# Optimization experiments

Measured on AMD Instinct MI355X. Metric: run time of the kernel, lower is better.

The kernel has to match this reference:

```python
import jax, jax.numpy as jnp
import numpy as np

FACTOR = 5  # module default


def setup_inputs() -> dict:
    key = jax.random.key(0)
    k1, k2, k3, k4 = jax.random.split(key, 4)
    B, L, H, D = 4, 2048, 8, 64
    S = min(FACTOR * int(np.ceil(np.log(L))), L)  # sample_k = U_part = 40
    return {
        "queries": jax.random.normal(k1, (B, L, H, D), jnp.float32),
        "keys": jax.random.normal(k2, (B, L, H, D), jnp.float32),
        "values": jax.random.normal(k3, (B, L, H, D), jnp.float32),
        "index_sample": jax.random.randint(k4, (L, S), 0, L, jnp.int32),
    }


def reference(queries, keys, values, index_sample):
    # queries/keys/values: [B, L, H, D]; index_sample: [L_Q, sample_k]
    B, L_Q, H, D = queries.shape
    L_K = keys.shape[1]
    Q = jnp.transpose(queries, (0, 2, 1, 3))  # [B,H,L_Q,D]
    K = jnp.transpose(keys, (0, 2, 1, 3))     # [B,H,L_K,D]
    V = jnp.transpose(values, (0, 2, 1, 3))   # [B,H,L_V,D]

    u = min(FACTOR * int(np.ceil(np.log(L_Q))), L_Q)  # n_top

    # --- _prob_QK: sampled QK scores (gather instead of materializing K_expand) ---
    K_sample = K[:, :, index_sample, :]                       # [B,H,L_Q,S,D]
    QK_sample = jnp.einsum('bhld,bhlsd->bhls', Q, K_sample)   # [B,H,L_Q,S]
    M = QK_sample.max(-1) - QK_sample.sum(-1) / L_K           # sparsity measure [B,H,L_Q]
    M_top = jax.lax.top_k(M, u)[1]                            # [B,H,u] query indices

    Q_reduce = jnp.take_along_axis(Q, M_top[..., None], axis=2)  # [B,H,u,D]
    scale = 1.0 / np.sqrt(D)
    scores = jnp.einsum('bhud,bhkd->bhuk', Q_reduce, K) * scale  # [B,H,u,L_K]

    # --- initial context (mask_flag=True -> cumsum of V) ---
    context = jnp.cumsum(V, axis=2)                           # [B,H,L_Q,D]

    attn = jax.nn.softmax(scores, axis=-1)
    upd = jnp.einsum('bhuk,bhkd->bhud', attn, V)              # [B,H,u,D]

    bi = jnp.arange(B)[:, None, None]
    hi = jnp.arange(H)[None, :, None]
    context = context.at[bi, hi, M_top].set(upd)              # scatter selected rows

    return jnp.transpose(context, (0, 2, 1, 3))               # [B,L_Q,H,D]
```

## Files before the change

kernel.cpp:

```cpp
#include <hip/hip_runtime.h>
#include <hip/hip_bf16.h>

#define L_SEQ 2048
#define NH 8
#define DIM 64
#define SS 40
#define UU 40
#define NHD (NH * DIM)

__global__ __launch_bounds__(256) void m_kernel(const float* __restrict__ Qg,
                                                const float* __restrict__ Kg,
                                                const int* __restrict__ idx,
                                                float* __restrict__ M) {
    int B = blockIdx.x;
    int bh = B & 31;
    int l  = (B >> 5) * 4 + (threadIdx.x >> 6);
    int lane = threadIdx.x & 63;
    int b = bh >> 3, h = bh & 7;
    int g = lane >> 3, c = lane & 7;

    const float* Qp = Qg + ((size_t)(b * L_SEQ + l) * NH + h) * DIM;
    const int* ip = idx + l * SS + g;
    int ki0 = ip[0], ki1 = ip[8], ki2 = ip[16], ki3 = ip[24], ki4 = ip[32];

    float4 q0 = *(const float4*)(Qp + 4 * c);
    float4 q1 = *(const float4*)(Qp + 32 + 4 * c);

    const float* Kbase = Kg + (size_t)b * L_SEQ * NHD + (size_t)h * DIM;
    const float* r0 = Kbase + (size_t)ki0 * NHD;
    const float* r1 = Kbase + (size_t)ki1 * NHD;
    const float* r2 = Kbase + (size_t)ki2 * NHD;
    const float* r3 = Kbase + (size_t)ki3 * NHD;
    const float* r4 = Kbase + (size_t)ki4 * NHD;

    float4 a0 = *(const float4*)(r0 + 4 * c), b0 = *(const float4*)(r0 + 32 + 4 * c);
    float4 a1 = *(const float4*)(r1 + 4 * c), b1 = *(const float4*)(r1 + 32 + 4 * c);
    float4 a2 = *(const float4*)(r2 + 4 * c), b2 = *(const float4*)(r2 + 32 + 4 * c);
    float4 a3 = *(const float4*)(r3 + 4 * c), b3 = *(const float4*)(r3 + 32 + 4 * c);
    float4 a4 = *(const float4*)(r4 + 4 * c), b4 = *(const float4*)(r4 + 32 + 4 * c);

#define DOT8(ka, kb, out) { \
    float d_ = ka.x * q0.x; \
    d_ = fmaf(ka.y, q0.y, d_); d_ = fmaf(ka.z, q0.z, d_); d_ = fmaf(ka.w, q0.w, d_); \
    d_ = fmaf(kb.x, q1.x, d_); d_ = fmaf(kb.y, q1.y, d_); \
    d_ = fmaf(kb.z, q1.z, d_); d_ = fmaf(kb.w, q1.w, d_); \
    d_ += __shfl_xor(d_, 1); d_ += __shfl_xor(d_, 2); d_ += __shfl_xor(d_, 4); \
    out = d_; }

    float d0, d1, d2, d3, d4;
    DOT8(a0, b0, d0); DOT8(a1, b1, d1); DOT8(a2, b2, d2);
    DOT8(a3, b3, d3); DOT8(a4, b4, d4);
#undef DOT8

    float mx = fmaxf(fmaxf(fmaxf(d0, d1), fmaxf(d2, d3)), d4);
    float sm = d0 + d1 + d2 + d3 + d4;
    #pragma unroll
    for (int off = 8; off < 64; off <<= 1) {
        mx = fmaxf(mx, __shfl_xor(mx, off));
        sm += __shfl_xor(sm, off);
    }
    if (lane == 0) M[(size_t)bh * L_SEQ + l] = mx - sm * (1.0f / (float)L_SEQ);
}

__global__ __launch_bounds__(256) void topk_radix_kernel(const float* __restrict__ M,
                                                         int* __restrict__ Mtop) {
    __shared__ unsigned hist[256];
    __shared__ unsigned suf[256];
    __shared__ int eq_list[64];
    __shared__ unsigned sh_bin, sh_need, sh_cnt, sh_eqc;
    int bh = blockIdx.x, tid = threadIdx.x;
    const float* Mrow = M + (size_t)bh * L_SEQ;
    int base = tid * 8;

    float4 a0 = *(const float4*)(Mrow + base);
    float4 a1 = *(const float4*)(Mrow + base + 4);
    float fv[8] = {a0.x, a0.y, a0.z, a0.w, a1.x, a1.y, a1.z, a1.w};
    unsigned key[8];
    #pragma unroll
    for (int j = 0; j < 8; ++j) {
        unsigned u = __float_as_uint(fv[j]);
        key[j] = (u & 0x80000000u) ? ~u : (u | 0x80000000u);
    }

    unsigned actmask = 0xffu;
    unsigned thresh = 0;
    int need = UU;

    #pragma unroll
    for (int shift = 24; shift >= 0; shift -= 8) {
        hist[tid] = 0;
        __syncthreads();
        #pragma unroll
        for (int j = 0; j < 8; ++j)
            if ((actmask >> j) & 1u)
                atomicAdd(&hist[(key[j] >> shift) & 0xffu], 1u);
        __syncthreads();
        if (tid < 64) {
            int b0 = tid * 4;
            unsigned h0 = hist[b0], h1 = hist[b0 + 1], h2 = hist[b0 + 2], h3 = hist[b0 + 3];
            unsigned loc = h0 + h1 + h2 + h3;
            unsigned s = loc;
            #pragma unroll
            for (int off = 1; off < 64; off <<= 1) {
                unsigned o = __shfl_down(s, off, 64);
                if (tid + off < 64) s += o;
            }
            unsigned tail = s - loc;
            suf[b0 + 3] = tail;
            suf[b0 + 2] = tail + h3;
            suf[b0 + 1] = tail + h3 + h2;
            suf[b0 + 0] = tail + h3 + h2 + h1;
        }
        __syncthreads();
        {
            int sb = (int)suf[tid];
            if (sb < need && sb + (int)hist[tid] >= need) {
                sh_bin = (unsigned)tid;
                sh_need = (unsigned)(need - sb);
            }
        }
        __syncthreads();
        unsigned Bb = sh_bin;
        need = (int)sh_need;
        thresh = (thresh << 8) | Bb;
        #pragma unroll
        for (int j = 0; j < 8; ++j)
            if ((actmask >> j) & 1u)
                if (((key[j] >> shift) & 0xffu) != Bb) actmask &= ~(1u << j);
        __syncthreads();
    }

    if (tid == 0) { sh_cnt = 0; sh_eqc = 0; }
    __syncthreads();
    int* op = Mtop + bh * UU;
    #pragma unroll
    for (int j = 0; j < 8; ++j) {
        if (key[j] > thresh) {
            unsigned p = atomicAdd(&sh_cnt, 1u);
            op[p] = base + j;
        } else if (key[j] == thresh) {
            unsigned p = atomicAdd(&sh_eqc, 1u);
            if (p < 64) eq_list[p] = base + j;
        }
    }
    __syncthreads();
    unsigned cnt = sh_cnt, eqc = sh_eqc;
    if ((int)eqc == need) {
        if (tid < (unsigned)need) op[cnt + tid] = eq_list[tid];
    } else if (tid == 0) {
        if (eqc <= 64u) {
            for (int t = 0; t < need; ++t) {
                int mi = t;
                for (int j = t + 1; j < (int)eqc; ++j)
                    if (eq_list[j] < eq_list[mi]) mi = j;
                int tmp = eq_list[t]; eq_list[t] = eq_list[mi]; eq_list[mi] = tmp;
                op[cnt + t] = eq_list[t];
            }
        } else {
            int taken = 0;
            for (int i = 0; i < L_SEQ && taken < need; ++i) {
                unsigned u = __float_as_uint(Mrow[i]);
                unsigned k = (u & 0x80000000u) ? ~u : (u | 0x80000000u);
                if (k == thresh) op[cnt + taken++] = i;
            }
        }
    }
}

__global__ __launch_bounds__(256) void attn_general(
    const float* __restrict__ Qg, const float* __restrict__ Kg,
    const float* __restrict__ Vg, const int* __restrict__ Mtop,
    float* __restrict__ pm, float* __restrict__ pl, float* __restrict__ pO,
    float* __restrict__ out, int nsplit, int direct) {
    __shared__ float qs[UU * DIM];
    __shared__ float ks[64 * 68];
    __shared__ float ps[UU * 68];
    __shared__ float mm[UU], ll[UU], al[UU];
    int bx = blockIdx.x;
    int bh = bx / nsplit, sp = bx - bh * nsplit;
    int b = bh >> 3, h = bh & 7;
    int tid = threadIdx.x;
    int cpb = 32 / nsplit;
    const int* mt = Mtop + bh * UU;

    for (int i = tid; i < UU * DIM / 8; i += 256) {
        int u = i >> 3, dv = (i & 7) * 8;
        int row = mt[u];
        const float* qp = Qg + ((size_t)(b * L_SEQ + row) * NH + h) * DIM + dv;
        *(float4*)&qs[u * DIM + dv]     = *(const float4*)qp;
        *(float4*)&qs[u * DIM + dv + 4] = *(const float4*)(qp + 4);
    }
    if (tid < UU) { mm[tid] = -INFINITY; ll[tid] = 0.f; }

    int d0 = (tid & 31) * 2, ugp = tid >> 5;
    float o0[5], o1[5];
    #pragma unroll
    for (int j = 0; j < 5; ++j) { o0[j] = 0.f; o1[j] = 0.f; }

    for (int c = 0; c < cpb; ++c) {
        int k0 = (sp * cpb + c) * 64;
        if (c) __syncthreads();
        for (int i = tid; i < 64 * DIM / 8; i += 256) {
            int r = i >> 3, dv = (i & 7) * 8;
            const float* kp = Kg + ((size_t)(b * L_SEQ + k0 + r) * NH + h) * DIM + dv;
            *(float4*)&ks[r * 68 + dv]     = *(const float4*)kp;
            *(float4*)&ks[r * 68 + dv + 4] = *(const float4*)(kp + 4);
        }
        __syncthreads();

        {
            int k = tid & 63, ug = tid >> 6;
            float acc[10];
            #pragma unroll
            for (int j = 0; j < 10; ++j) acc[j] = 0.f;
            for (int d = 0; d < DIM; d += 4) {
                float4 kv = *(float4*)&ks[k * 68 + d];
                #pragma unroll
                for (int j = 0; j < 10; ++j) {
                    float4 qv = *(float4*)&qs[(ug * 10 + j) * DIM + d];
                    acc[j] = fmaf(qv.x, kv.x, acc[j]);
                    acc[j] = fmaf(qv.y, kv.y, acc[j]);
                    acc[j] = fmaf(qv.z, kv.z, acc[j]);
                    acc[j] = fmaf(qv.w, kv.w, acc[j]);
                }
            }
            #pragma unroll
            for (int j = 0; j < 10; ++j) ps[(ug * 10 + j) * 68 + k] = acc[j] * 0.125f;
        }
        __syncthreads();

        for (int i = tid; i < 64 * DIM / 8; i += 256) {
            int r = i >> 3, dv = (i & 7) * 8;
            const float* vp = Vg + ((size_t)(b * L_SEQ + k0 + r) * NH + h) * DIM + dv;
            *(float4*)&ks[r * 68 + dv]     = *(const float4*)vp;
            *(float4*)&ks[r * 68 + dv + 4] = *(const float4*)(vp + 4);
        }
        if (tid < UU) {
            float mc = -INFINITY;
            for (int k = 0; k < 64; ++k) mc = fmaxf(mc, ps[tid * 68 + k]);
            float mn = fmaxf(mm[tid], mc);
            float a = __expf(mm[tid] - mn);
            float s = 0.f;
            for (int k = 0; k < 64; ++k) {
                float e = __expf(ps[tid * 68 + k] - mn);
                ps[tid * 68 + k] = e;
                s += e;
            }
            ll[tid] = ll[tid] * a + s;
            mm[tid] = mn;
            al[tid] = a;
        }
        __syncthreads();

        {
            #pragma unroll
            for (int j = 0; j < 5; ++j) {
                float a = al[ugp * 5 + j];
                o0[j] *= a; o1[j] *= a;
            }
            for (int k = 0; k < 64; k += 4) {
                float vf0[4], vf1[4];
                #pragma unroll
                for (int kk = 0; kk < 4; ++kk) {
                    float2 vv = *(float2*)&ks[(k + kk) * 68 + d0];
                    vf0[kk] = vv.x;
                    vf1[kk] = vv.y;
                }
                #pragma unroll
                for (int j = 0; j < 5; ++j) {
                    float4 pv = *(float4*)&ps[(ugp * 5 + j) * 68 + k];
                    o0[j] = fmaf(pv.x, vf0[0], o0[j]); o1[j] = fmaf(pv.x, vf1[0], o1[j]);
                    o0[j] = fmaf(pv.y, vf0[1], o0[j]); o1[j] = fmaf(pv.y, vf1[1], o1[j]);
                    o0[j] = fmaf(pv.z, vf0[2], o0[j]); o1[j] = fmaf(pv.z, vf1[2], o1[j]);
                    o0[j] = fmaf(pv.w, vf0[3], o0[j]); o1[j] = fmaf(pv.w, vf1[3], o1[j]);
                }
            }
        }
    }

    if (!direct) {
        if (tid < UU) {
            pm[((size_t)bh * nsplit + sp) * UU + tid] = mm[tid];
            pl[((size_t)bh * nsplit + sp) * UU + tid] = ll[tid];
        }
        size_t basep = ((size_t)bh * nsplit + sp) * UU * DIM;
        #pragma unroll
        for (int j = 0; j < 5; ++j) {
            *(float2*)&pO[basep + (size_t)(ugp * 5 + j) * DIM + d0] = make_float2(o0[j], o1[j]);
        }
    } else {
        #pragma unroll
        for (int j = 0; j < 5; ++j) {
            int u = ugp * 5 + j;
            int row = mt[u];
            float inv = 1.0f / ll[u];
            size_t o = ((size_t)(b * L_SEQ + row) * NH + h) * DIM + d0;
            out[o]     = o0[j] * inv;
            out[o + 1] = o1[j] * inv;
        }
    }
}

__global__ __launch_bounds__(256) void csum8_kernel(const float* __restrict__ Vg,
                                                    float* __restrict__ cs8) {
    int wid = blockIdx.x * 4 + (threadIdx.x >> 6);
    int lane = threadIdx.x & 63;
    int c8 = wid & 255, bh = wid >> 8;
    int b = bh >> 3, h = bh & 7;
    const float* Vp = Vg + ((size_t)(b * L_SEQ + c8 * 8) * NH + h) * DIM + lane;
    float s = 0.f;
    #pragma unroll
    for (int j = 0; j < 8; ++j) s += Vp[(size_t)j * NHD];
    cs8[((size_t)bh * 256 + c8) * 64 + lane] = s;
}

__global__ __launch_bounds__(256) void prefix8_kernel(float* __restrict__ cs8) {
    __shared__ float buf[256 * 64];
    int bh = blockIdx.x, tid = threadIdx.x;
    float* g = cs8 + (size_t)bh * 16384;
    for (int it = 0; it < 16; ++it) {
        int i = it * 1024 + tid * 4;
        *(float4*)&buf[i] = *(const float4*)&g[i];
    }
    __syncthreads();
    if (tid < 64) {
        float run = 0.f;
        for (int c = 0; c < 256; ++c) {
            float t = buf[c * 64 + tid];
            buf[c * 64 + tid] = run;
            run += t;
        }
    }
    __syncthreads();
    for (int it = 0; it < 16; ++it) {
        int i = it * 1024 + tid * 4;
        *(float4*)&g[i] = *(const float4*)&buf[i];
    }
}

__global__ __launch_bounds__(256) void csum_write8_kernel(const float* __restrict__ Vg,
                                                          const float* __restrict__ cs8,
                                                          float* __restrict__ out) {
    int wid = blockIdx.x * 4 + (threadIdx.x >> 6);
    int lane = threadIdx.x & 63;
    int c8 = wid & 255, bh = wid >> 8;
    int b = bh >> 3, h = bh & 7;
    float run = cs8[((size_t)bh * 256 + c8) * 64 + lane];
    size_t off = ((size_t)(b * L_SEQ + c8 * 8) * NH + h) * DIM + lane;
    const float* Vp = Vg + off;
    float* Op = out + off;
    #pragma unroll
    for (int j = 0; j < 8; ++j) {
        run += Vp[(size_t)j * NHD];
        Op[(size_t)j * NHD] = run;
    }
}

__global__ __launch_bounds__(256) void csum_fused_kernel(const float* __restrict__ Vg,
                                                         float* __restrict__ out) {
    __shared__ float css[32 * 64];
    int bh = blockIdx.x, tid = threadIdx.x;
    int b = bh >> 3, h = bh & 7;
    int cc = tid >> 3, d8 = (tid & 7) * 8;
    size_t off = ((size_t)(b * L_SEQ + cc * 64) * NH + h) * DIM + d8;
    const float* Vp = Vg + off;
    float s[8];
    #pragma unroll
    for (int j = 0; j < 8; ++j) s[j] = 0.f;
    for (int l = 0; l < 64; ++l) {
        float4 r0 = *(const float4*)(Vp + (size_t)l * NHD);
        float4 r1 = *(const float4*)(Vp + (size_t)l * NHD + 4);
        s[0] += r0.x; s[1] += r0.y; s[2] += r0.z; s[3] += r0.w;
        s[4] += r1.x; s[5] += r1.y; s[6] += r1.z; s[7] += r1.w;
    }
    #pragma unroll
    for (int j = 0; j < 8; ++j) css[cc * 64 + d8 + j] = s[j];
    __syncthreads();
    if (tid < 64) {
        float run = 0.f;
        for (int c = 0; c < 32; ++c) {
            float t = css[c * 64 + tid];
            css[c * 64 + tid] = run;
            run += t;
        }
    }
    __syncthreads();
    float r8[8];
    #pragma unroll
    for (int j = 0; j < 8; ++j) r8[j] = css[cc * 64 + d8 + j];
    float* Op = out + off;
    for (int l = 0; l < 64; ++l) {
        float4 r0 = *(const float4*)(Vp + (size_t)l * NHD);
        float4 r1 = *(const float4*)(Vp + (size_t)l * NHD + 4);
        r8[0] += r0.x; r8[1] += r0.y; r8[2] += r0.z; r8[3] += r0.w;
        r8[4] += r1.x; r8[5] += r1.y; r8[6] += r1.z; r8[7] += r1.w;
        *(float4*)(Op + (size_t)l * NHD)     = make_float4(r8[0], r8[1], r8[2], r8[3]);
        *(float4*)(Op + (size_t)l * NHD + 4) = make_float4(r8[4], r8[5], r8[6], r8[7]);
    }
}

__global__ __launch_bounds__(256) void combine_kernel(
    const float* __restrict__ pm, const float* __restrict__ pl,
    const float* __restrict__ pO, const int* __restrict__ Mtop,
    float* __restrict__ out, int nsplit) {
    int wid = blockIdx.x * 4 + (threadIdx.x >> 6);
    int lane = threadIdx.x & 63;
    int u = wid % UU;
    int bh = wid / UU;
    int b = bh >> 3, h = bh & 7;
    float mg = -INFINITY;
    for (int c = 0; c < nsplit; ++c) mg = fmaxf(mg, pm[((size_t)bh * nsplit + c) * UU + u]);
    float acc = 0.f, lsum = 0.f;
    for (int c = 0; c < nsplit; ++c) {
        size_t pb = ((size_t)bh * nsplit + c) * UU + u;
        float w = __expf(pm[pb] - mg);
        lsum = fmaf(pl[pb], w, lsum);
        acc = fmaf(w, pO[pb * DIM + lane], acc);
    }
    int row = Mtop[bh * UU + u];
    out[((size_t)(b * L_SEQ + row) * NH + h) * DIM + lane] = acc / lsum;
}

extern "C" void kernel_launch(void* const* d_in, const int* in_sizes, int n_in,
                              void* d_out, int out_size, void* d_ws, size_t ws_size,
                              hipStream_t stream) {
    const float* Q = (const float*)d_in[0];
    const float* K = (const float*)d_in[1];
    const float* V = (const float*)d_in[2];
    const int* idx = (const int*)d_in[3];
    float* out = (float*)d_out;
    float* wsf = (float*)d_ws;

    int n = 0;
    const int cands[5] = {32, 16, 8, 4, 2};
    for (int i = 0; i < 5; ++i) {
        size_t need = (size_t)(591104 + 84480 * cands[i]) * 4;
        if (ws_size >= need) { n = cands[i]; break; }
    }

    if (n > 0) {
        float* M    = wsf;
        int*   Mtop = (int*)(wsf + 65536);
        float* pm   = wsf + 66816;
        float* pl   = pm + 1280 * (size_t)n;
        float* pO   = pl + 1280 * (size_t)n;
        float* cs8  = pO + 81920 * (size_t)n;
        m_kernel<<<16384, 256, 0, stream>>>(Q, K, idx, M);
        topk_radix_kernel<<<32, 256, 0, stream>>>(M, Mtop);
        attn_general<<<32 * n, 256, 0, stream>>>(Q, K, V, Mtop, pm, pl, pO, out, n, 0);
        csum8_kernel<<<2048, 256, 0, stream>>>(V, cs8);
        prefix8_kernel<<<32, 256, 0, stream>>>(cs8);
        csum_write8_kernel<<<2048, 256, 0, stream>>>(V, cs8, out);
        combine_kernel<<<320, 256, 0, stream>>>(pm, pl, pO, Mtop, out, n);
    } else if (ws_size >= (size_t)(66816 + 524288) * 4) {
        float* M    = wsf;
        int*   Mtop = (int*)(wsf + 65536);
        float* cs8  = wsf + 66816;
        m_kernel<<<16384, 256, 0, stream>>>(Q, K, idx, M);
        topk_radix_kernel<<<32, 256, 0, stream>>>(M, Mtop);
        csum8_kernel<<<2048, 256, 0, stream>>>(V, cs8);
        prefix8_kernel<<<32, 256, 0, stream>>>(cs8);
        csum_write8_kernel<<<2048, 256, 0, stream>>>(V, cs8, out);
        attn_general<<<32, 256, 0, stream>>>(Q, K, V, Mtop, nullptr, nullptr, nullptr, out, 1, 1);
    } else {
        float* M    = (float*)d_out;
        int*   Mtop = (int*)d_ws;
        m_kernel<<<16384, 256, 0, stream>>>(Q, K, idx, M);
        topk_radix_kernel<<<32, 256, 0, stream>>>(M, Mtop);
        csum_fused_kernel<<<32, 256, 0, stream>>>(V, out);
        attn_general<<<32, 256, 0, stream>>>(Q, K, V, Mtop, nullptr, nullptr, nullptr, out, 1, 1);
    }
}
```

Measured before the change: 191.4 us.

## Merge independent kernels into three heterogeneous stages and remap M computation

Independent work is grouped into shared launches by block-index range: M scoring with the V chunk sums, top-k selection with the chunk prefix scan, and sampled attention with the cumulative-sum write-out. This cuts the launch count from seven to four and lets independent work share the GPU. The M kernel is also remapped so each wavefront covers all 8 heads for one query position and loops over the 40 samples, giving contiguous K-row reads across heads. The cost is fewer blocks for the M stage, more serial work per wave, and larger shared-memory footprints in the combined kernels, which can lower occupancy.

```diff
diff --git a/kernel.cpp b/kernel.cpp
--- a/kernel.cpp
+++ b/kernel.cpp
@@ -1,44 +1,30 @@
 #include <hip/hip_runtime.h>
-#include <hip/hip_bf16.h>
 
 #define L_SEQ 2048
 #define NH 8
 #define DIM 64
 #define SS 40
 #define UU 40
-#define NHD (NH * DIM)
-
-__global__ __launch_bounds__(256) void m_kernel(const float* __restrict__ Qg,
-                                                const float* __restrict__ Kg,
-                                                const int* __restrict__ idx,
-                                                float* __restrict__ M) {
-    int B = blockIdx.x;
-    int bh = B & 31;
-    int l  = (B >> 5) * 4 + (threadIdx.x >> 6);
-    int lane = threadIdx.x & 63;
-    int b = bh >> 3, h = bh & 7;
-    int g = lane >> 3, c = lane & 7;
-
-    const float* Qp = Qg + ((size_t)(b * L_SEQ + l) * NH + h) * DIM;
-    const int* ip = idx + l * SS + g;
-    int ki0 = ip[0], ki1 = ip[8], ki2 = ip[16], ki3 = ip[24], ki4 = ip[32];
-
-    float4 q0 = *(const float4*)(Qp + 4 * c);
-    float4 q1 = *(const float4*)(Qp + 32 + 4 * c);
-
-    const float* Kbase = Kg + (size_t)b * L_SEQ * NHD + (size_t)h * DIM;
-    const float* r0 = Kbase + (size_t)ki0 * NHD;
-    const float* r1 = Kbase + (size_t)ki1 * NHD;
-    const float* r2 = Kbase + (size_t)ki2 * NHD;
-    const float* r3 = Kbase + (size_t)ki3 * NHD;
-    const float* r4 = Kbase + (size_t)ki4 * NHD;
-
-    float4 a0 = *(const float4*)(r0 + 4 * c), b0 = *(const float4*)(r0 + 32 + 4 * c);
-    float4 a1 = *(const float4*)(r1 + 4 * c), b1 = *(const float4*)(r1 + 32 + 4 * c);
-    float4 a2 = *(const float4*)(r2 + 4 * c), b2 = *(const float4*)(r2 + 32 + 4 * c);
-    float4 a3 = *(const float4*)(r3 + 4 * c), b3 = *(const float4*)(r3 + 32 + 4 * c);
-    float4 a4 = *(const float4*)(r4 + 4 * c), b4 = *(const float4*)(r4 + 32 + 4 * c);
-
+#define NHD 512
+
+
+__device__ __forceinline__ void m_body(const float* __restrict__ Qg,
+                                       const float* __restrict__ Kg,
+                                       const int* __restrict__ idx,
+                                       float* __restrict__ M,
+                                       int bx, int tid) {
+    int lane = tid & 63;
+    int b = bx & 3;
+    int l = (bx >> 2) * 4 + (tid >> 6);
+    int h = lane >> 3, c = lane & 7;
+
+    const float* Qp = Qg + ((size_t)(b * L_SEQ + l) * NH + h) * DIM + c * 8;
+    float4 q0 = *(const float4*)Qp;
+    float4 q1 = *(const float4*)(Qp + 4);
+    const float* Kbase = Kg + (size_t)b * L_SEQ * NHD + h * DIM + c * 8;
+    const int* ip = idx + l * SS;
+
+    float mx = -INFINITY, sm = 0.f;
 #define DOT8(ka, kb, out) { \
     float d_ = ka.x * q0.x; \
     d_ = fmaf(ka.y, q0.y, d_); d_ = fmaf(ka.z, q0.z, d_); d_ = fmaf(ka.w, q0.w, d_); \
@@ -46,140 +32,67 @@
     d_ = fmaf(kb.z, q1.z, d_); d_ = fmaf(kb.w, q1.w, d_); \
     d_ += __shfl_xor(d_, 1); d_ += __shfl_xor(d_, 2); d_ += __shfl_xor(d_, 4); \
     out = d_; }
-
-    float d0, d1, d2, d3, d4;
-    DOT8(a0, b0, d0); DOT8(a1, b1, d1); DOT8(a2, b2, d2);
-    DOT8(a3, b3, d3); DOT8(a4, b4, d4);
+    #pragma unroll
+    for (int s = 0; s < SS; s += 5) {
+        int k0 = ip[s], k1 = ip[s+1], k2 = ip[s+2], k3 = ip[s+3], k4 = ip[s+4];
+        const float* r0 = Kbase + (size_t)k0 * NHD;
+        const float* r1 = Kbase + (size_t)k1 * NHD;
+        const float* r2 = Kbase + (size_t)k2 * NHD;
+        const float* r3 = Kbase + (size_t)k3 * NHD;
+        const float* r4 = Kbase + (size_t)k4 * NHD;
+        float4 a0 = *(const float4*)r0, b0 = *(const float4*)(r0 + 4);
+        float4 a1 = *(const float4*)r1, b1 = *(const float4*)(r1 + 4);
+        float4 a2 = *(const float4*)r2, b2 = *(const float4*)(r2 + 4);
+        float4 a3 = *(const float4*)r3, b3 = *(const float4*)(r3 + 4);
+        float4 a4 = *(const float4*)r4, b4 = *(const float4*)(r4 + 4);
+        float d0, d1, d2, d3, d4;
+        DOT8(a0, b0, d0); DOT8(a1, b1, d1); DOT8(a2, b2, d2);
+        DOT8(a3, b3, d3); DOT8(a4, b4, d4);
+        mx = fmaxf(mx, fmaxf(fmaxf(d0, d1), fmaxf(fmaxf(d2, d3), d4)));
+        sm += d0 + d1 + d2 + d3 + d4;
+    }
 #undef DOT8
-
-    float mx = fmaxf(fmaxf(fmaxf(d0, d1), fmaxf(d2, d3)), d4);
-    float sm = d0 + d1 + d2 + d3 + d4;
-    #pragma unroll
-    for (int off = 8; off < 64; off <<= 1) {
-        mx = fmaxf(mx, __shfl_xor(mx, off));
-        sm += __shfl_xor(sm, off);
-    }
-    if (lane == 0) M[(size_t)bh * L_SEQ + l] = mx - sm * (1.0f / (float)L_SEQ);
-}
-
-__global__ __launch_bounds__(256) void topk_radix_kernel(const float* __restrict__ M,
-                                                         int* __restrict__ Mtop) {
-    __shared__ unsigned hist[256];
-    __shared__ unsigned suf[256];
-    __shared__ int eq_list[64];
-    __shared__ unsigned sh_bin, sh_need, sh_cnt, sh_eqc;
-    int bh = blockIdx.x, tid = threadIdx.x;
-    const float* Mrow = M + (size_t)bh * L_SEQ;
-    int base = tid * 8;
-
-    float4 a0 = *(const float4*)(Mrow + base);
-    float4 a1 = *(const float4*)(Mrow + base + 4);
-    float fv[8] = {a0.x, a0.y, a0.z, a0.w, a1.x, a1.y, a1.z, a1.w};
-    unsigned key[8];
+    if (c == 0) M[((size_t)(b * NH + h)) * L_SEQ + l] = mx - sm * (1.0f / (float)L_SEQ);
+}
+
+__device__ __forceinline__ void csum8_body(const float* __restrict__ Vg,
+                                           float* __restrict__ cs8,
+                                           int wid, int lane) {
+    int c8 = wid & 255, bh = wid >> 8;
+    int b = bh >> 3, h = bh & 7;
+    const float* Vp = Vg + ((size_t)(b * L_SEQ + c8 * 8) * NH + h) * DIM + lane;
+    float s = 0.f;
+    #pragma unroll
+    for (int j = 0; j < 8; ++j) s += Vp[(size_t)j * NHD];
+    cs8[((size_t)bh * 256 + c8) * 64 + lane] = s;
+}
+
+__device__ __forceinline__ void write8_body(const float* __restrict__ Vg,
+                                            const float* __restrict__ cs8,
+                                            float* __restrict__ out,
+                                            int wid, int lane) {
+    int c8 = wid & 255, bh = wid >> 8;
+    int b = bh >> 3, h = bh & 7;
+    float run = cs8[((size_t)bh * 256 + c8) * 64 + lane];
+    size_t off = ((size_t)(b * L_SEQ + c8 * 8) * NH + h) * DIM + lane;
+    const float* Vp = Vg + off;
+    float* Op = out + off;
     #pragma unroll
     for (int j = 0; j < 8; ++j) {
-        unsigned u = __float_as_uint(fv[j]);
-        key[j] = (u & 0x80000000u) ? ~u : (u | 0x80000000u);
-    }
-
-    unsigned actmask = 0xffu;
-    unsigned thresh = 0;
-    int need = UU;
-
-    #pragma unroll
-    for (int shift = 24; shift >= 0; shift -= 8) {
-        hist[tid] = 0;
-        __syncthreads();
-        #pragma unroll
-        for (int j = 0; j < 8; ++j)
-            if ((actmask >> j) & 1u)
-                atomicAdd(&hist[(key[j] >> shift) & 0xffu], 1u);
-        __syncthreads();
-        if (tid < 64) {
-            int b0 = tid * 4;
-            unsigned h0 = hist[b0], h1 = hist[b0 + 1], h2 = hist[b0 + 2], h3 = hist[b0 + 3];
-            unsigned loc = h0 + h1 + h2 + h3;
-            unsigned s = loc;
-            #pragma unroll
-            for (int off = 1; off < 64; off <<= 1) {
-                unsigned o = __shfl_down(s, off, 64);
-                if (tid + off < 64) s += o;
-            }
-            unsigned tail = s - loc;
-            suf[b0 + 3] = tail;
-            suf[b0 + 2] = tail + h3;
-            suf[b0 + 1] = tail + h3 + h2;
-            suf[b0 + 0] = tail + h3 + h2 + h1;
-        }
-        __syncthreads();
-        {
-            int sb = (int)suf[tid];
-            if (sb < need && sb + (int)hist[tid] >= need) {
-                sh_bin = (unsigned)tid;
-                sh_need = (unsigned)(need - sb);
-            }
-        }
-        __syncthreads();
-        unsigned Bb = sh_bin;
-        need = (int)sh_need;
-        thresh = (thresh << 8) | Bb;
-        #pragma unroll
-        for (int j = 0; j < 8; ++j)
-            if ((actmask >> j) & 1u)
-                if (((key[j] >> shift) & 0xffu) != Bb) actmask &= ~(1u << j);
-        __syncthreads();
-    }
-
-    if (tid == 0) { sh_cnt = 0; sh_eqc = 0; }
-    __syncthreads();
-    int* op = Mtop + bh * UU;
-    #pragma unroll
-    for (int j = 0; j < 8; ++j) {
-        if (key[j] > thresh) {
-            unsigned p = atomicAdd(&sh_cnt, 1u);
-            op[p] = base + j;
-        } else if (key[j] == thresh) {
-            unsigned p = atomicAdd(&sh_eqc, 1u);
-            if (p < 64) eq_list[p] = base + j;
-        }
-    }
-    __syncthreads();
-    unsigned cnt = sh_cnt, eqc = sh_eqc;
-    if ((int)eqc == need) {
-        if (tid < (unsigned)need) op[cnt + tid] = eq_list[tid];
-    } else if (tid == 0) {
-        if (eqc <= 64u) {
-            for (int t = 0; t < need; ++t) {
-                int mi = t;
-                for (int j = t + 1; j < (int)eqc; ++j)
-                    if (eq_list[j] < eq_list[mi]) mi = j;
-                int tmp = eq_list[t]; eq_list[t] = eq_list[mi]; eq_list[mi] = tmp;
-                op[cnt + t] = eq_list[t];
-            }
-        } else {
-            int taken = 0;
-            for (int i = 0; i < L_SEQ && taken < need; ++i) {
-                unsigned u = __float_as_uint(Mrow[i]);
-                unsigned k = (u & 0x80000000u) ? ~u : (u | 0x80000000u);
-                if (k == thresh) op[cnt + taken++] = i;
-            }
-        }
-    }
-}
-
-__global__ __launch_bounds__(256) void attn_general(
-    const float* __restrict__ Qg, const float* __restrict__ Kg,
-    const float* __restrict__ Vg, const int* __restrict__ Mtop,
-    float* __restrict__ pm, float* __restrict__ pl, float* __restrict__ pO,
-    float* __restrict__ out, int nsplit, int direct) {
-    __shared__ float qs[UU * DIM];
-    __shared__ float ks[64 * 68];
-    __shared__ float ps[UU * 68];
-    __shared__ float mm[UU], ll[UU], al[UU];
-    int bx = blockIdx.x;
+        run += Vp[(size_t)j * NHD];
+        Op[(size_t)j * NHD] = run;
+    }
+}
+
+__device__ void attn_body(const float* __restrict__ Qg, const float* __restrict__ Kg,
+                          const float* __restrict__ Vg, const int* __restrict__ Mtop,
+                          float* __restrict__ pm, float* __restrict__ pl,
+                          float* __restrict__ pO, float* __restrict__ out,
+                          int nsplit, int direct, int bx, int tid,
+                          float* qs, float* ks, float* ps,
+                          float* mm, float* ll, float* al) {
     int bh = bx / nsplit, sp = bx - bh * nsplit;
     int b = bh >> 3, h = bh & 7;
-    int tid = threadIdx.x;
     int cpb = 32 / nsplit;
     const int* mt = Mtop + bh * UU;
 
@@ -301,108 +214,196 @@
     }
 }
 
-__global__ __launch_bounds__(256) void csum8_kernel(const float* __restrict__ Vg,
-                                                    float* __restrict__ cs8) {
-    int wid = blockIdx.x * 4 + (threadIdx.x >> 6);
-    int lane = threadIdx.x & 63;
-    int c8 = wid & 255, bh = wid >> 8;
-    int b = bh >> 3, h = bh & 7;
-    const float* Vp = Vg + ((size_t)(b * L_SEQ + c8 * 8) * NH + h) * DIM + lane;
-    float s = 0.f;
-    #pragma unroll
-    for (int j = 0; j < 8; ++j) s += Vp[(size_t)j * NHD];
-    cs8[((size_t)bh * 256 + c8) * 64 + lane] = s;
-}
-
-__global__ __launch_bounds__(256) void prefix8_kernel(float* __restrict__ cs8) {
+
+__global__ __launch_bounds__(256) void stage1_kernel(const float* __restrict__ Qg,
+                                                     const float* __restrict__ Kg,
+                                                     const int* __restrict__ idx,
+                                                     const float* __restrict__ Vg,
+                                                     float* __restrict__ M,
+                                                     float* __restrict__ cs8) {
+    int bx = blockIdx.x, tid = threadIdx.x;
+    if (bx < 2048) {
+        m_body(Qg, Kg, idx, M, bx, tid);
+    } else {
+        int wid = (bx - 2048) * 4 + (tid >> 6);
+        csum8_body(Vg, cs8, wid, tid & 63);
+    }
+}
+
+__global__ __launch_bounds__(256) void stage2_kernel(const float* __restrict__ M,
+                                                     int* __restrict__ Mtop,
+                                                     float* __restrict__ cs8) {
+    __shared__ unsigned hist[256];
+    __shared__ unsigned suf[256];
+    __shared__ int eq_list[64];
+    __shared__ unsigned sh_bin, sh_need, sh_cnt, sh_eqc;
     __shared__ float buf[256 * 64];
-    int bh = blockIdx.x, tid = threadIdx.x;
-    float* g = cs8 + (size_t)bh * 16384;
-    for (int it = 0; it < 16; ++it) {
-        int i = it * 1024 + tid * 4;
-        *(float4*)&buf[i] = *(const float4*)&g[i];
-    }
-    __syncthreads();
-    if (tid < 64) {
-        float run = 0.f;
-        for (int c = 0; c < 256; ++c) {
-            float t = buf[c * 64 + tid];
-            buf[c * 64 + tid] = run;
-            run += t;
-        }
-    }
-    __syncthreads();
-    for (int it = 0; it < 16; ++it) {
-        int i = it * 1024 + tid * 4;
-        *(float4*)&g[i] = *(const float4*)&buf[i];
-    }
-}
-
-__global__ __launch_bounds__(256) void csum_write8_kernel(const float* __restrict__ Vg,
-                                                          const float* __restrict__ cs8,
-                                                          float* __restrict__ out) {
-    int wid = blockIdx.x * 4 + (threadIdx.x >> 6);
-    int lane = threadIdx.x & 63;
-    int c8 = wid & 255, bh = wid >> 8;
-    int b = bh >> 3, h = bh & 7;
-    float run = cs8[((size_t)bh * 256 + c8) * 64 + lane];
-    size_t off = ((size_t)(b * L_SEQ + c8 * 8) * NH + h) * DIM + lane;
-    const float* Vp = Vg + off;
-    float* Op = out + off;
-    #pragma unroll
-    for (int j = 0; j < 8; ++j) {
-        run += Vp[(size_t)j * NHD];
-        Op[(size_t)j * NHD] = run;
-    }
-}
-
-__global__ __launch_bounds__(256) void csum_fused_kernel(const float* __restrict__ Vg,
-                                                         float* __restrict__ out) {
-    __shared__ float css[32 * 64];
-    int bh = blockIdx.x, tid = threadIdx.x;
-    int b = bh >> 3, h = bh & 7;
-    int cc = tid >> 3, d8 = (tid & 7) * 8;
-    size_t off = ((size_t)(b * L_SEQ + cc * 64) * NH + h) * DIM + d8;
-    const float* Vp = Vg + off;
-    float s[8];
-    #pragma unroll
-    for (int j = 0; j < 8; ++j) s[j] = 0.f;
-    for (int l = 0; l < 64; ++l) {
-        float4 r0 = *(const float4*)(Vp + (size_t)l * NHD);
-        float4 r1 = *(const float4*)(Vp + (size_t)l * NHD + 4);
-        s[0] += r0.x; s[1] += r0.y; s[2] += r0.z; s[3] += r0.w;
-        s[4] += r1.x; s[5] += r1.y; s[6] += r1.z; s[7] += r1.w;
-    }
-    #pragma unroll
-    for (int j = 0; j < 8; ++j) css[cc * 64 + d8 + j] = s[j];
-    __syncthreads();
-    if (tid < 64) {
-        float run = 0.f;
-        for (int c = 0; c < 32; ++c) {
-            float t = css[c * 64 + tid];
-            css[c * 64 + tid] = run;
-            run += t;
-        }
-    }
-    __syncthreads();
-    float r8[8];
-    #pragma unroll
-    for (int j = 0; j < 8; ++j) r8[j] = css[cc * 64 + d8 + j];
-    float* Op = out + off;
-    for (int l = 0; l < 64; ++l) {
-        float4 r0 = *(const float4*)(Vp + (size_t)l * NHD);
-        float4 r1 = *(const float4*)(Vp + (size_t)l * NHD + 4);
-        r8[0] += r0.x; r8[1] += r0.y; r8[2] += r0.z; r8[3] += r0.w;
-        r8[4] += r1.x; r8[5] += r1.y; r8[6] += r1.z; r8[7] += r1.w;
-        *(float4*)(Op + (size_t)l * NHD)     = make_float4(r8[0], r8[1], r8[2], r8[3]);
-        *(float4*)(Op + (size_t)l * NHD + 4) = make_float4(r8[4], r8[5], r8[6], r8[7]);
-    }
-}
-
-__global__ __launch_bounds__(256) void combine_kernel(
-    const float* __restrict__ pm, const float* __restrict__ pl,
-    const float* __restrict__ pO, const int* __restrict__ Mtop,
-    float* __restrict__ out, int nsplit) {
+    int bx = blockIdx.x, tid = threadIdx.x;
+
+    if (bx < 32) {
+        int bh = bx;
+        const float* Mrow = M + (size_t)bh * L_SEQ;
+        int base = tid * 8;
+        float4 a0 = *(const float4*)(Mrow + base);
+        float4 a1 = *(const float4*)(Mrow + base + 4);
+        float fv[8] = {a0.x, a0.y, a0.z, a0.w, a1.x, a1.y, a1.z, a1.w};
+        unsigned key[8];
+        #pragma unroll
+        for (int j = 0; j < 8; ++j) {
+            unsigned u = __float_as_uint(fv[j]);
+            key[j] = (u & 0x80000000u) ? ~u : (u | 0x80000000u);
+        }
+        unsigned actmask = 0xffu;
+        unsigned thresh = 0;
+        int need = UU;
+        #pragma unroll
+        for (int shift = 24; shift >= 0; shift -= 8) {
+            hist[tid] = 0;
+            __syncthreads();
+            #pragma unroll
+            for (int j = 0; j < 8; ++j)
+                if ((actmask >> j) & 1u)
+                    atomicAdd(&hist[(key[j] >> shift) & 0xffu], 1u);
+            __syncthreads();
+            if (tid < 64) {
+                int b0 = tid * 4;
+                unsigned h0 = hist[b0], h1 = hist[b0 + 1], h2 = hist[b0 + 2], h3 = hist[b0 + 3];
+                unsigned loc = h0 + h1 + h2 + h3;
+                unsigned s = loc;
+                #pragma unroll
+                for (int off = 1; off < 64; off <<= 1) {
+                    unsigned o = __shfl_down(s, off, 64);
+                    if (tid + off < 64) s += o;
+                }
+                unsigned tail = s - loc;
+                suf[b0 + 3] = tail;
+                suf[b0 + 2] = tail + h3;
+                suf[b0 + 1] = tail + h3 + h2;
+                suf[b0 + 0] = tail + h3 + h2 + h1;
+            }
+            __syncthreads();
+            {
+                int sb = (int)suf[tid];
+                if (sb < need && sb + (int)hist[tid] >= need) {
+                    sh_bin = (unsigned)tid;
+                    sh_need = (unsigned)(need - sb);
+                }
+            }
+            __syncthreads();
+            unsigned Bb = sh_bin;
+            need = (int)sh_need;
+            thresh = (thresh << 8) | Bb;
+            #pragma unroll
+            for (int j = 0; j < 8; ++j)
+                if ((actmask >> j) & 1u)
+                    if (((key[j] >> shift) & 0xffu) != Bb) actmask &= ~(1u << j);
+            __syncthreads();
+        }
+        if (tid == 0) { sh_cnt = 0; sh_eqc = 0; }
+        __syncthreads();
+        int* op = Mtop + bh * UU;
+        #pragma unroll
+        for (int j = 0; j < 8; ++j) {
+            if (key[j] > thresh) {
+                unsigned p = atomicAdd(&sh_cnt, 1u);
+                op[p] = base + j;
+            } else if (key[j] == thresh) {
+                unsigned p = atomicAdd(&sh_eqc, 1u);
+                if (p < 64) eq_list[p] = base + j;
+            }
+        }
+        __syncthreads();
+        unsigned cnt = sh_cnt, eqc = sh_eqc;
+        if ((int)eqc == need) {
+            if (tid < (unsigned)need) op[cnt + tid] = eq_list[tid];
+        } else if (tid == 0) {
+            if (eqc <= 64u) {
+                for (int t = 0; t < need; ++t) {
+                    int mi = t;
+                    for (int j = t + 1; j < (int)eqc; ++j)
+                        if (eq_list[j] < eq_list[mi]) mi = j;
+                    int tmp = eq_list[t]; eq_list[t] = eq_list[mi]; eq_list[mi] = tmp;
+                    op[cnt + t] = eq_list[t];
+                }
+            } else {
+                int taken = 0;
+                for (int i = 0; i < L_SEQ && taken < need; ++i) {
+                    unsigned u = __float_as_uint(Mrow[i]);
+                    unsigned k = (u & 0x80000000u) ? ~u : (u | 0x80000000u);
+                    if (k == thresh) op[cnt + taken++] = i;
+                }
+            }
+        }
+    } else {
+        int bh = bx - 32;
+        float* g = cs8 + (size_t)bh * 16384;
+        for (int it = 0; it < 16; ++it) {
+            int i = it * 1024 + tid * 4;
+            *(float4*)&buf[i] = *(const float4*)&g[i];
+        }
+        __syncthreads();
+        if (tid < 64) {
+            float run = 0.f;
+            for (int c = 0; c < 256; ++c) {
+                float t = buf[c * 64 + tid];
+                buf[c * 64 + tid] = run;
+                run += t;
+            }
+        }
+        __syncthreads();
+        for (int it = 0; it < 16; ++it) {
+            int i = it * 1024 + tid * 4;
+            *(float4*)&g[i] = *(const float4*)&buf[i];
+        }
+    }
+}
+
+__global__ __launch_bounds__(256) void stage3_kernel(const float* __restrict__ Qg,
+                                                     const float* __restrict__ Kg,
+                                                     const float* __restrict__ Vg,
+                                                     const int* __restrict__ Mtop,
+                                                     const float* __restrict__ cs8,
+                                                     float* __restrict__ pm,
+                                                     float* __restrict__ pl,
+                                                     float* __restrict__ pO,
+                                                     float* __restrict__ out,
+                                                     int nattn, int nsplit) {
+    __shared__ float qs[UU * DIM];
+    __shared__ float ks[64 * 68];
+    __shared__ float ps[UU * 68];
+    __shared__ float mm[UU], ll[UU], al[UU];
+    int bx = blockIdx.x, tid = threadIdx.x;
+    if (bx < nattn) {
+        attn_body(Qg, Kg, Vg, Mtop, pm, pl, pO, out, nsplit, 0, bx, tid,
+                  qs, ks, ps, mm, ll, al);
+    } else {
+        int wid = (bx - nattn) * 4 + (tid >> 6);
+        write8_body(Vg, cs8, out, wid, tid & 63);
+    }
+}
+
+__global__ __launch_bounds__(256) void attn_kernel(const float* __restrict__ Qg,
+                                                   const float* __restrict__ Kg,
+                                                   const float* __restrict__ Vg,
+                                                   const int* __restrict__ Mtop,
+                                                   float* __restrict__ pm,
+                                                   float* __restrict__ pl,
+                                                   float* __restrict__ pO,
+                                                   float* __restrict__ out,
+                                                   int nsplit, int direct) {
+    __shared__ float qs[UU * DIM];
+    __shared__ float ks[64 * 68];
+    __shared__ float ps[UU * 68];
+    __shared__ float mm[UU], ll[UU], al[UU];
+    attn_body(Qg, Kg, Vg, Mtop, pm, pl, pO, out, nsplit, direct,
+              blockIdx.x, threadIdx.x, qs, ks, ps, mm, ll, al);
+}
+
+__global__ __launch_bounds__(256) void combine_kernel(const float* __restrict__ pm,
+                                                      const float* __restrict__ pl,
+                                                      const float* __restrict__ pO,
+                                                      const int* __restrict__ Mtop,
+                                                      float* __restrict__ out, int nsplit) {
     int wid = blockIdx.x * 4 + (threadIdx.x >> 6);
     int lane = threadIdx.x & 63;
     int u = wid % UU;
@@ -421,6 +422,49 @@
     out[((size_t)(b * L_SEQ + row) * NH + h) * DIM + lane] = acc / lsum;
 }
 
+__global__ __launch_bounds__(256) void csum_fused_kernel(const float* __restrict__ Vg,
+                                                         float* __restrict__ out) {
+    __shared__ float css[32 * 64];
+    int bh = blockIdx.x, tid = threadIdx.x;
+    int b = bh >> 3, h = bh & 7;
+    int cc = tid >> 3, d8 = (tid & 7) * 8;
+    size_t off = ((size_t)(b * L_SEQ + cc * 64) * NH + h) * DIM + d8;
+    const float* Vp = Vg + off;
+    float s[8];
+    #pragma unroll
+    for (int j = 0; j < 8; ++j) s[j] = 0.f;
+    for (int l = 0; l < 64; ++l) {
+        float4 r0 = *(const float4*)(Vp + (size_t)l * NHD);
+        float4 r1 = *(const float4*)(Vp + (size_t)l * NHD + 4);
+        s[0] += r0.x; s[1] += r0.y; s[2] += r0.z; s[3] += r0.w;
+        s[4] += r1.x; s[5] += r1.y; s[6] += r1.z; s[7] += r1.w;
+    }
+    #pragma unroll
+    for (int j = 0; j < 8; ++j) css[cc * 64 + d8 + j] = s[j];
+    __syncthreads();
+    if (tid < 64) {
+        float run = 0.f;
+        for (int c = 0; c < 32; ++c) {
+            float t = css[c * 64 + tid];
+            css[c * 64 + tid] = run;
+            run += t;
+        }
+    }
+    __syncthreads();
+    float r8[8];
+    #pragma unroll
+    for (int j = 0; j < 8; ++j) r8[j] = css[cc * 64 + d8 + j];
+    float* Op = out + off;
+    for (int l = 0; l < 64; ++l) {
+        float4 r0 = *(const float4*)(Vp + (size_t)l * NHD);
+        float4 r1 = *(const float4*)(Vp + (size_t)l * NHD + 4);
+        r8[0] += r0.x; r8[1] += r0.y; r8[2] += r0.z; r8[3] += r0.w;
+        r8[4] += r1.x; r8[5] += r1.y; r8[6] += r1.z; r8[7] += r1.w;
+        *(float4*)(Op + (size_t)l * NHD)     = make_float4(r8[0], r8[1], r8[2], r8[3]);
+        *(float4*)(Op + (size_t)l * NHD + 4) = make_float4(r8[4], r8[5], r8[6], r8[7]);
+    }
+}
+
 extern "C" void kernel_launch(void* const* d_in, const int* in_sizes, int n_in,
                               void* d_out, int out_size, void* d_ws, size_t ws_size,
                               hipStream_t stream) {
@@ -445,29 +489,28 @@
         float* pl   = pm + 1280 * (size_t)n;
         float* pO   = pl + 1280 * (size_t)n;
         float* cs8  = pO + 81920 * (size_t)n;
-        m_kernel<<<16384, 256, 0, stream>>>(Q, K, idx, M);
-        topk_radix_kernel<<<32, 256, 0, stream>>>(M, Mtop);
-        attn_general<<<32 * n, 256, 0, stream>>>(Q, K, V, Mtop, pm, pl, pO, out, n, 0);
-        csum8_kernel<<<2048, 256, 0, stream>>>(V, cs8);
-        prefix8_kernel<<<32, 256, 0, stream>>>(cs8);
-        csum_write8_kernel<<<2048, 256, 0, stream>>>(V, cs8, out);
+        stage1_kernel<<<4096, 256, 0, stream>>>(Q, K, idx, V, M, cs8);
+        stage2_kernel<<<64, 256, 0, stream>>>(M, Mtop, cs8);
+        stage3_kernel<<<32 * n + 2048, 256, 0, stream>>>(Q, K, V, Mtop, cs8,
+                                                         pm, pl, pO, out, 32 * n, n);
         combine_kernel<<<320, 256, 0, stream>>>(pm, pl, pO, Mtop, out, n);
     } else if (ws_size >= (size_t)(66816 + 524288) * 4) {
         float* M    = wsf;
         int*   Mtop = (int*)(wsf + 65536);
         float* cs8  = wsf + 66816;
-        m_kernel<<<16384, 256, 0, stream>>>(Q, K, idx, M);
-        topk_radix_kernel<<<32, 256, 0, stream>>>(M, Mtop);
-        csum8_kernel<<<2048, 256, 0, stream>>>(V, cs8);
-        prefix8_kernel<<<32, 256, 0, stream>>>(cs8);
-        csum_write8_kernel<<<2048, 256, 0, stream>>>(V, cs8, out);
-        attn_general<<<32, 256, 0, stream>>>(Q, K, V, Mtop, nullptr, nullptr, nullptr, out, 1, 1);
+        stage1_kernel<<<4096, 256, 0, stream>>>(Q, K, idx, V, M, cs8);
+        stage2_kernel<<<64, 256, 0, stream>>>(M, Mtop, cs8);
+        stage3_kernel<<<2048, 256, 0, stream>>>(Q, K, V, Mtop, cs8,
+                                                nullptr, nullptr, nullptr, out, 0, 1);
+        attn_kernel<<<32, 256, 0, stream>>>(Q, K, V, Mtop, nullptr, nullptr, nullptr,
+                                            out, 1, 1);
     } else {
         float* M    = (float*)d_out;
         int*   Mtop = (int*)d_ws;
-        m_kernel<<<16384, 256, 0, stream>>>(Q, K, idx, M);
-        topk_radix_kernel<<<32, 256, 0, stream>>>(M, Mtop);
+        stage1_kernel<<<2048, 256, 0, stream>>>(Q, K, idx, nullptr, M, nullptr);
+        stage2_kernel<<<32, 256, 0, stream>>>(M, Mtop, nullptr);
         csum_fused_kernel<<<32, 256, 0, stream>>>(V, out);
-        attn_general<<<32, 256, 0, stream>>>(Q, K, V, Mtop, nullptr, nullptr, nullptr, out, 1, 1);
-    }
-}
+        attn_kernel<<<32, 256, 0, stream>>>(Q, K, V, Mtop, nullptr, nullptr, nullptr,
+                                            out, 1, 1);
+    }
+}
```

New measurement: 177.7 us. -7.2%, faster.
